# Kernel optimization log

Measured on AMD Instinct MI355X. Metric: run time of the kernel, lower is better.

The kernel has to match this reference:

```python
import jax, jax.numpy as jnp
import numpy as np
import itertools

# ---- fixed problem dims ----
B, C, G, D, H, W_SP = 2, 32, 24, 24, 24, 24   # octahedral group |G| = 24 (isomorphic to S4)
N_SEL = 3                                      # selective bispectrum: 2nd shift restricted to {e, transposition, 4-cycle}
FEAT = G * N_SEL                               # 72 invariant features per channel
HEAD = 64


def _octahedral_tables():
    """Cayley table of the octahedral rotation group (== S4) and the selective generator set."""
    perms = list(itertools.permutations(range(4)))          # lexicographic; identity at index 0
    idx = {p: i for i, p in enumerate(perms)}
    # cayley[i, j] = index of p_i o p_j, with (p o q)(k) = p(q(k))
    cay = np.array([[idx[tuple(p[q[k]] for k in range(4))] for q in perms] for p in perms],
                   dtype=np.int32)
    sel = np.array([idx[(0, 1, 2, 3)],   # identity
                    idx[(1, 0, 2, 3)],   # transposition (generator)
                    idx[(1, 2, 3, 0)]],  # 4-cycle (generator)
                   dtype=np.int32)
    return cay, sel


def setup_inputs() -> dict:
    key = jax.random.key(0)
    k1, k2, k3 = jax.random.split(key, 3)
    x = jax.random.normal(k1, (B, C, G, D, H, W_SP), dtype=jnp.float32)
    cay, sel = _octahedral_tables()
    # 1x1x1 Conv3d params: weight (HEAD, C*FEAT), bias (HEAD,)
    fan_in = C * FEAT
    W = jax.random.normal(k2, (HEAD, fan_in), dtype=jnp.float32) * (1.0 / np.sqrt(fan_in))
    b = jax.random.normal(k3, (HEAD,), dtype=jnp.float32) * 0.01
    return {"x": x, "W": W, "b": b,
            "cayley": jnp.asarray(cay), "sel_idx": jnp.asarray(sel)}


def _bispectrum_pool(x, W, b, cayley, sel_idx):
    Bb, Cc, Gg, Dd, Hh, Ww = x.shape
    # (B,C,G,D,H,W) -> rows of group signals, one per (b,c,voxel)
    xf = x.astype(jnp.float32).transpose(0, 1, 3, 4, 5, 2).reshape(-1, Gg)   # (N, 24)
    N = xf.shape[0]
    # Selective triple correlation (bispectrum in group domain):
    #   tau[n, h, s] = sum_g f(g) * f(g.h) * f(g.s),  s in selective generator set
    tau = jnp.zeros((N, Gg, N_SEL), dtype=jnp.float32)
    for g in range(Gg):                      # fixed small loop over 24 group elements
        row = cayley[g]                      # (24,) indices of g.h for all h
        fgh = xf[:, row]                     # (N, 24)
        fgs = fgh[:, sel_idx]                # (N, 3)
        tau = tau + xf[:, g][:, None, None] * fgh[:, :, None] * fgs[:, None, :]
    beta = tau.reshape(N, FEAT)              # real part of the bispectrum
    # sign * log1p compression
    out = jnp.sign(beta) * jnp.log1p(jnp.abs(beta))
    # (N, FEAT) -> (B, C*FEAT, D, H, W), channel index = c*FEAT + f (matches torch permute/reshape)
    out = out.reshape(Bb, Cc, Dd, Hh, Ww, FEAT).transpose(0, 1, 5, 2, 3, 4)
    out = out.reshape(Bb, Cc * FEAT, Dd, Hh, Ww)
    out = jax.nn.relu(out)
    # 1x1x1 conv == per-voxel GEMM
    y = jnp.einsum('bkdhw,ok->bodhw', out, W) + b[None, :, None, None, None]
    return y


def reference(x, W, b, cayley, sel_idx):
    return _bispectrum_pool(x, W, b, cayley, sel_idx)
```

## Files before the change

### kernel.cpp

```cpp
#include <hip/hip_runtime.h>
#include <stdint.h>

#define DHW         13824
#define NCH         32
#define NG          24
#define FEATC       72
#define KDIM        2304
#define NHEAD       64
#define TP          16
#define CHS         16
#define KPE         1160
#define TILES_PER_B 864
#define NTILES      1728
#define KSTEPS      72
#define KSTG        36
#define KQ          9
#define OUTN        1769472
#define WS_WBS      294912
#define WS_NEED     (WS_WBS + 2u * OUTN * 4u)

typedef __attribute__((ext_vector_type(2))) float    f32x2;
typedef __attribute__((ext_vector_type(8))) short    s16x8;
typedef __attribute__((ext_vector_type(4))) float    f32x4;
typedef __attribute__((ext_vector_type(4))) uint32_t u32x4;

struct Tables { int cay[NG][NG]; int s1[NG]; int s2[NG]; };

constexpr Tables make_tables() {
    int perms[NG][4] = {};
    int n = 0;
    for (int a = 0; a < 4; ++a)
        for (int b = 0; b < 4; ++b) {
            if (b == a) continue;
            for (int c = 0; c < 4; ++c) {
                if (c == a || c == b) continue;
                int d = 6 - a - b - c;
                perms[n][0] = a; perms[n][1] = b; perms[n][2] = c; perms[n][3] = d;
                ++n;
            }
        }
    int si1 = 0, si2 = 0;
    for (int i = 0; i < NG; ++i) {
        if (perms[i][0] == 1 && perms[i][1] == 0 && perms[i][2] == 2 && perms[i][3] == 3) si1 = i;
        if (perms[i][0] == 1 && perms[i][1] == 2 && perms[i][2] == 3 && perms[i][3] == 0) si2 = i;
    }
    Tables t{};
    for (int p = 0; p < NG; ++p) {
        for (int q = 0; q < NG; ++q) {
            int c0 = perms[p][perms[q][0]];
            int c1 = perms[p][perms[q][1]];
            int c2 = perms[p][perms[q][2]];
            int c3 = perms[p][perms[q][3]];
            int r = 0;
            for (int i = 0; i < NG; ++i)
                if (perms[i][0] == c0 && perms[i][1] == c1 &&
                    perms[i][2] == c2 && perms[i][3] == c3) { r = i; break; }
            t.cay[p][q] = r;
        }
        t.s1[p] = t.cay[p][si1];
        t.s2[p] = t.cay[p][si2];
    }
    return t;
}
constexpr Tables TAB = make_tables();

__device__ __forceinline__ uint32_t f2bf(float f) {
    uint32_t u = __float_as_uint(f);
    u += 0x7fffu + ((u >> 16) & 1u);
    return u >> 16;
}

__global__ __launch_bounds__(256) void prep_w(const float* __restrict__ W,
                                              unsigned short* __restrict__ WbS) {
    int i = blockIdx.x * 256 + threadIdx.x;
    if (i >= NHEAD * KDIM) return;
    int j  = i & 7;
    int t1 = i >> 3;
    int l  = t1 & 63;
    int t2 = t1 >> 6;
    int kk = t2 % KSTEPS;
    int ot = t2 / KSTEPS;
    int o = ot * 16 + (l & 15);
    int k = kk * 32 + ((l >> 4) << 3) + j;
    WbS[i] = (unsigned short)f2bf(W[o * KDIM + k] * 0.69314718055994531f);
}

__global__ __launch_bounds__(256) void reduce_y(const float* __restrict__ part,
                                                const float* __restrict__ bias,
                                                float* __restrict__ y) {
    const int i4 = blockIdx.x * 256 + threadIdx.x;
    const f32x4 v0 = ((const f32x4*)part)[i4];
    const f32x4 v1 = ((const f32x4*)(part + OUTN))[i4];
    const float b  = bias[((i4 * 4) / DHW) & (NHEAD - 1)];
    f32x4 r = v0 + v1;
    r[0] += b; r[1] += b; r[2] += b; r[3] += b;
    ((f32x4*)y)[i4] = r;
}

template<int SPLIT>
__global__ __launch_bounds__(256, 2)
void bispec_fused(
        const float* __restrict__ x,
        const unsigned short* __restrict__ WbS,
        const float* __restrict__ bias,
        float* __restrict__ out)
{
    __shared__ alignas(16) unsigned short featS[TP * KPE];

    const int bid = blockIdx.x;
    const int NB  = SPLIT ? NTILES * 2 : NTILES;
    const int swz   = (bid & 7) * (NB / 8) + (bid >> 3);
    const int tile  = SPLIT ? (swz % NTILES) : swz;
    const int sbeg  = SPLIT ? (swz / NTILES) : 0;
    const int send  = SPLIT ? sbeg + 1 : 2;
    const int bb  = tile / TILES_PER_B;
    const int psp = (tile - bb * TILES_PER_B) * TP;
    const int tid = threadIdx.x;

    const int p0 = tid & 15;
    const int cl = tid >> 4;
    const int w  = tid >> 6;
    const int l  = tid & 63;
    const int ln = l & 15;
    const int lh = l >> 4;

    f32x4 accA = {0.f, 0.f, 0.f, 0.f};
    f32x4 accB = {0.f, 0.f, 0.f, 0.f};
    f32x4 accC = {0.f, 0.f, 0.f, 0.f};
    f32x4 accD = {0.f, 0.f, 0.f, 0.f};

    #pragma unroll 1
    for (int stage = sbeg; stage < send; ++stage) {
        {
            const int c0 = stage * CHS + cl;
            const unsigned idx0 = (unsigned)(bb * NCH + c0) * (NG * DHW) + (unsigned)(psp + p0);
            float xf[NG];
            #pragma unroll
            for (int g = 0; g < NG; ++g) xf[g] = x[idx0 + (unsigned)(g * DHW)];

            float tau0[NG];
            f32x2 tau12[NG];
            #pragma unroll
            for (int h = 0; h < NG; ++h) { tau0[h] = 0.f; tau12[h] = (f32x2){0.f, 0.f}; }
            #pragma unroll
            for (int g = 0; g < NG; ++g) {
                const float xg = xf[g];
                const float q0 = xg * xg;
                const f32x2 q12 = {xg * xf[TAB.s1[g]], xg * xf[TAB.s2[g]]};
                #pragma unroll
                for (int h = 0; h < NG; ++h) {
                    const float v = xf[TAB.cay[g][h]];
                    tau0[h] = fmaf(q0, v, tau0[h]);
                    tau12[h] = __builtin_elementwise_fma((f32x2){v, v}, q12, tau12[h]);
                }
            }
            uint32_t pk[FEATC / 2];
            #pragma unroll
            for (int h = 0; h < NG; h += 2) {
                float f0 = __log2f(1.f + fmaxf(tau0[h],       0.f));
                float f1 = __log2f(1.f + fmaxf(tau12[h][0],   0.f));
                float f2 = __log2f(1.f + fmaxf(tau12[h][1],   0.f));
                float f3 = __log2f(1.f + fmaxf(tau0[h+1],     0.f));
                float f4 = __log2f(1.f + fmaxf(tau12[h+1][0], 0.f));
                float f5 = __log2f(1.f + fmaxf(tau12[h+1][1], 0.f));
                const int bw = (h >> 1) * 3;
                pk[bw + 0] = f2bf(f0) | (f2bf(f1) << 16);
                pk[bw + 1] = f2bf(f2) | (f2bf(f3) << 16);
                pk[bw + 2] = f2bf(f4) | (f2bf(f5) << 16);
            }
            uint32_t* dst = (uint32_t*)&featS[p0 * KPE + cl * FEATC];
            #pragma unroll
            for (int i = 0; i < FEATC / 2; i += 4) {
                u32x4 v; v[0] = pk[i]; v[1] = pk[i+1]; v[2] = pk[i+2]; v[3] = pk[i+3];
                *(u32x4*)(dst + i) = v;
            }
        }
        __syncthreads();

        {
            const unsigned kbase = (unsigned)(stage * KSTG + w * KQ);
            const unsigned short* fb = &featS[ln * KPE + (w * KQ) * 32 + lh * 8];
            const s16x8* wb = (const s16x8*)WbS;

            s16x8 bc = *(const s16x8*)(fb);
            #pragma unroll
            for (int kk = 0; kk < KQ; ++kk) {
                s16x8 bn = bc;
                if (kk + 1 < KQ) bn = *(const s16x8*)(fb + (kk + 1) * 32);
                const unsigned ai = (kbase + (unsigned)kk) * 64u + (unsigned)l;
                s16x8 a0 = wb[ai];
                s16x8 a1 = wb[ai + 1u * KSTEPS * 64u];
                s16x8 a2 = wb[ai + 2u * KSTEPS * 64u];
                s16x8 a3 = wb[ai + 3u * KSTEPS * 64u];
                accA = __builtin_amdgcn_mfma_f32_16x16x32_bf16(a0, bc, accA, 0, 0, 0);
                accB = __builtin_amdgcn_mfma_f32_16x16x32_bf16(a1, bc, accB, 0, 0, 0);
                accC = __builtin_amdgcn_mfma_f32_16x16x32_bf16(a2, bc, accC, 0, 0, 0);
                accD = __builtin_amdgcn_mfma_f32_16x16x32_bf16(a3, bc, accD, 0, 0, 0);
                bc = bn;
            }
        }
        __syncthreads();
    }

    f32x4* redS = (f32x4*)featS;
    redS[(w * 4 + 0) * 64 + l] = accA;
    redS[(w * 4 + 1) * 64 + l] = accB;
    redS[(w * 4 + 2) * 64 + l] = accC;
    redS[(w * 4 + 3) * 64 + l] = accD;
    __syncthreads();
    f32x4 r = redS[(0 * 4 + w) * 64 + l] + redS[(1 * 4 + w) * 64 + l]
            + redS[(2 * 4 + w) * 64 + l] + redS[(3 * 4 + w) * 64 + l];

    const size_t obase = (SPLIT ? (size_t)sbeg * OUTN : 0)
                       + (size_t)bb * NHEAD * DHW + (size_t)(psp + ln);
    #pragma unroll
    for (int j = 0; j < 4; ++j) {
        const int o = w * 16 + lh * 4 + j;
        const float bv = SPLIT ? 0.f : bias[o];
        out[obase + (size_t)o * DHW] = r[j] + bv;
    }
}

extern "C" void kernel_launch(void* const* d_in, const int* in_sizes, int n_in,
                              void* d_out, int out_size, void* d_ws, size_t ws_size,
                              hipStream_t stream) {
    const float* x    = (const float*)d_in[0];
    const float* W    = (const float*)d_in[1];
    const float* bias = (const float*)d_in[2];
    unsigned short* WbS = (unsigned short*)d_ws;
    float* part = (float*)((char*)d_ws + WS_WBS);

    prep_w<<<dim3((NHEAD * KDIM + 255) / 256), dim3(256), 0, stream>>>(W, WbS);
    if (ws_size >= (size_t)WS_NEED) {
        bispec_fused<1><<<dim3(NTILES * 2), dim3(256), 0, stream>>>(x, WbS, bias, part);
        reduce_y<<<dim3(OUTN / 4 / 256), dim3(256), 0, stream>>>(part, bias, (float*)d_out);
    } else {
        bispec_fused<0><<<dim3(NTILES), dim3(256), 0, stream>>>(x, WbS, bias, (float*)d_out);
    }
}
```

Before: 70.59 us.

## Exploit transposition symmetry to drop duplicate bispectrum features and fold into weights

The transposition-shift bispectrum component satisfies tau[h,t] = tau[t·h,t], so only 12 of its 24 values are unique. The kernel now computes those 12 values and folds the matching weight columns by summing them in prep_w. Per-channel features go from 72 to 60, padded to 64, so the GEMM K dimension shrinks from 2304 to 2048. This cuts FMA, log and MFMA work and simplifies weight-index math, at the cost of slightly different bf16 rounding of the summed weights.

```diff
diff --git a/kernel.cpp b/kernel.cpp
--- a/kernel.cpp
+++ b/kernel.cpp
@@ -4,17 +4,19 @@
 #define DHW         13824
 #define NCH         32
 #define NG          24
-#define FEATC       72
 #define KDIM        2304
 #define NHEAD       64
 #define TP          16
 #define CHS         16
-#define KPE         1160
+#define NFC         60
+#define FPC         64
+#define KP2         2048
+#define KS2         64
+#define KPSTG       32
+#define KQ          8
+#define KPE         1032
 #define TILES_PER_B 864
 #define NTILES      1728
-#define KSTEPS      72
-#define KSTG        36
-#define KQ          9
 #define OUTN        1769472
 #define WS_WBS      294912
 #define WS_NEED     (WS_WBS + 2u * OUTN * 4u)
@@ -24,7 +26,7 @@
 typedef __attribute__((ext_vector_type(4))) float    f32x4;
 typedef __attribute__((ext_vector_type(4))) uint32_t u32x4;
 
-struct Tables { int cay[NG][NG]; int s1[NG]; int s2[NG]; };
+struct Tables { int cay[NG][NG]; int s1[NG]; int s2[NG]; int t1h[NG]; int rep[12]; };
 
 constexpr Tables make_tables() {
     int perms[NG][4] = {};
@@ -60,6 +62,9 @@
         t.s1[p] = t.cay[p][si1];
         t.s2[p] = t.cay[p][si2];
     }
+    for (int h = 0; h < NG; ++h) t.t1h[h] = t.cay[si1][h];
+    int nr = 0;
+    for (int h = 0; h < NG; ++h) if (h < t.t1h[h]) t.rep[nr++] = h;
     return t;
 }
 constexpr Tables TAB = make_tables();
@@ -73,16 +78,24 @@
 __global__ __launch_bounds__(256) void prep_w(const float* __restrict__ W,
                                               unsigned short* __restrict__ WbS) {
     int i = blockIdx.x * 256 + threadIdx.x;
-    if (i >= NHEAD * KDIM) return;
     int j  = i & 7;
-    int t1 = i >> 3;
-    int l  = t1 & 63;
-    int t2 = t1 >> 6;
-    int kk = t2 % KSTEPS;
-    int ot = t2 / KSTEPS;
+    int t1_ = i >> 3;
+    int l  = t1_ & 63;
+    int t2_ = t1_ >> 6;
+    int kk = t2_ & (KS2 - 1);
+    int ot = t2_ >> 6;
     int o = ot * 16 + (l & 15);
     int k = kk * 32 + ((l >> 4) << 3) + j;
-    WbS[i] = (unsigned short)f2bf(W[o * KDIM + k] * 0.69314718055994531f);
+    int stage = k >> 10;
+    int q     = k & 1023;
+    int c = stage * CHS + (q >> 6);
+    int f = q & 63;
+    const float* Wo = W + o * KDIM + c * 72;
+    float val = 0.f;
+    if (f < 24)      val = Wo[f * 3 + 0];
+    else if (f < 36) { int h = TAB.rep[f - 24]; val = Wo[h * 3 + 1] + Wo[TAB.t1h[h] * 3 + 1]; }
+    else if (f < 60) { int h = f - 36;          val = Wo[h * 3 + 2]; }
+    WbS[i] = (unsigned short)f2bf(val * 0.69314718055994531f);
 }
 
 __global__ __launch_bounds__(256) void reduce_y(const float* __restrict__ part,
@@ -138,39 +151,51 @@
             #pragma unroll
             for (int g = 0; g < NG; ++g) xf[g] = x[idx0 + (unsigned)(g * DHW)];
 
-            float tau0[NG];
-            f32x2 tau12[NG];
-            #pragma unroll
-            for (int h = 0; h < NG; ++h) { tau0[h] = 0.f; tau12[h] = (f32x2){0.f, 0.f}; }
+            f32x2 tau02[NG];
+            float tau1[12];
+            #pragma unroll
+            for (int h = 0; h < NG; ++h) tau02[h] = (f32x2){0.f, 0.f};
+            #pragma unroll
+            for (int r = 0; r < 12; ++r) tau1[r] = 0.f;
             #pragma unroll
             for (int g = 0; g < NG; ++g) {
                 const float xg = xf[g];
-                const float q0 = xg * xg;
-                const f32x2 q12 = {xg * xf[TAB.s1[g]], xg * xf[TAB.s2[g]]};
+                const f32x2 q02 = (f32x2){xg, xg} * (f32x2){xg, xf[TAB.s2[g]]};
+                const float q1 = xg * xf[TAB.s1[g]];
                 #pragma unroll
                 for (int h = 0; h < NG; ++h) {
                     const float v = xf[TAB.cay[g][h]];
-                    tau0[h] = fmaf(q0, v, tau0[h]);
-                    tau12[h] = __builtin_elementwise_fma((f32x2){v, v}, q12, tau12[h]);
+                    tau02[h] = __builtin_elementwise_fma((f32x2){v, v}, q02, tau02[h]);
                 }
-            }
-            uint32_t pk[FEATC / 2];
-            #pragma unroll
-            for (int h = 0; h < NG; h += 2) {
-                float f0 = __log2f(1.f + fmaxf(tau0[h],       0.f));
-                float f1 = __log2f(1.f + fmaxf(tau12[h][0],   0.f));
-                float f2 = __log2f(1.f + fmaxf(tau12[h][1],   0.f));
-                float f3 = __log2f(1.f + fmaxf(tau0[h+1],     0.f));
-                float f4 = __log2f(1.f + fmaxf(tau12[h+1][0], 0.f));
-                float f5 = __log2f(1.f + fmaxf(tau12[h+1][1], 0.f));
-                const int bw = (h >> 1) * 3;
-                pk[bw + 0] = f2bf(f0) | (f2bf(f1) << 16);
-                pk[bw + 1] = f2bf(f2) | (f2bf(f3) << 16);
-                pk[bw + 2] = f2bf(f4) | (f2bf(f5) << 16);
-            }
-            uint32_t* dst = (uint32_t*)&featS[p0 * KPE + cl * FEATC];
-            #pragma unroll
-            for (int i = 0; i < FEATC / 2; i += 4) {
+                #pragma unroll
+                for (int r = 0; r < 12; ++r) {
+                    const float v = xf[TAB.cay[g][TAB.rep[r]]];
+                    tau1[r] = fmaf(q1, v, tau1[r]);
+                }
+            }
+            uint32_t pk[FPC / 2];
+            #pragma unroll
+            for (int i = 0; i < 12; ++i) {
+                float a = __log2f(1.f + fmaxf(tau02[2*i][0],   0.f));
+                float b = __log2f(1.f + fmaxf(tau02[2*i+1][0], 0.f));
+                pk[i] = f2bf(a) | (f2bf(b) << 16);
+            }
+            #pragma unroll
+            for (int i = 0; i < 6; ++i) {
+                float a = __log2f(1.f + fmaxf(tau1[2*i],   0.f));
+                float b = __log2f(1.f + fmaxf(tau1[2*i+1], 0.f));
+                pk[12 + i] = f2bf(a) | (f2bf(b) << 16);
+            }
+            #pragma unroll
+            for (int i = 0; i < 12; ++i) {
+                float a = __log2f(1.f + fmaxf(tau02[2*i][1],   0.f));
+                float b = __log2f(1.f + fmaxf(tau02[2*i+1][1], 0.f));
+                pk[18 + i] = f2bf(a) | (f2bf(b) << 16);
+            }
+            pk[30] = 0u; pk[31] = 0u;
+            uint32_t* dst = (uint32_t*)&featS[p0 * KPE + cl * FPC];
+            #pragma unroll
+            for (int i = 0; i < FPC / 2; i += 4) {
                 u32x4 v; v[0] = pk[i]; v[1] = pk[i+1]; v[2] = pk[i+2]; v[3] = pk[i+3];
                 *(u32x4*)(dst + i) = v;
             }
@@ -178,7 +203,7 @@
         __syncthreads();
 
         {
-            const unsigned kbase = (unsigned)(stage * KSTG + w * KQ);
+            const unsigned kb = (unsigned)(stage * KPSTG + w * KQ);
             const unsigned short* fb = &featS[ln * KPE + (w * KQ) * 32 + lh * 8];
             const s16x8* wb = (const s16x8*)WbS;
 
@@ -187,11 +212,11 @@
             for (int kk = 0; kk < KQ; ++kk) {
                 s16x8 bn = bc;
                 if (kk + 1 < KQ) bn = *(const s16x8*)(fb + (kk + 1) * 32);
-                const unsigned ai = (kbase + (unsigned)kk) * 64u + (unsigned)l;
+                const unsigned ai = (kb + (unsigned)kk) * 64u + (unsigned)l;
                 s16x8 a0 = wb[ai];
-                s16x8 a1 = wb[ai + 1u * KSTEPS * 64u];
-                s16x8 a2 = wb[ai + 2u * KSTEPS * 64u];
-                s16x8 a3 = wb[ai + 3u * KSTEPS * 64u];
+                s16x8 a1 = wb[ai + 1u * KS2 * 64u];
+                s16x8 a2 = wb[ai + 2u * KS2 * 64u];
+                s16x8 a3 = wb[ai + 3u * KS2 * 64u];
                 accA = __builtin_amdgcn_mfma_f32_16x16x32_bf16(a0, bc, accA, 0, 0, 0);
                 accB = __builtin_amdgcn_mfma_f32_16x16x32_bf16(a1, bc, accB, 0, 0, 0);
                 accC = __builtin_amdgcn_mfma_f32_16x16x32_bf16(a2, bc, accC, 0, 0, 0);
@@ -230,7 +255,7 @@
     unsigned short* WbS = (unsigned short*)d_ws;
     float* part = (float*)((char*)d_ws + WS_WBS);
 
-    prep_w<<<dim3((NHEAD * KDIM + 255) / 256), dim3(256), 0, stream>>>(W, WbS);
+    prep_w<<<dim3(NHEAD * KP2 / 256), dim3(256), 0, stream>>>(W, WbS);
     if (ws_size >= (size_t)WS_NEED) {
         bispec_fused<1><<<dim3(NTILES * 2), dim3(256), 0, stream>>>(x, WbS, bias, part);
         reduce_y<<<dim3(OUTN / 4 / 256), dim3(256), 0, stream>>>(part, bias, (float*)d_out);
```

Result: faster. 61.93 us (-12.3%).
